# Performance work log

Measured on AMD Instinct MI355X. Metric: run time of the kernel, lower is better.

Reference implementation:

```python
import jax, jax.numpy as jnp
import numpy as np

N = 1_000_000
D_IN = 64
D_HID = 128
NUM_SEG = 8192


def setup_inputs() -> dict:
    key = jax.random.key(0)
    ks = jax.random.split(key, 8)
    f_all = jax.random.normal(ks[0], (N, D_IN), dtype=jnp.float32)
    seg_ids = jnp.sort(jax.random.randint(ks[1], (N,), 0, NUM_SEG, dtype=jnp.int32))
    W1 = jax.random.normal(ks[2], (D_IN, 32), dtype=jnp.float32) * 0.1
    b1 = jax.random.normal(ks[3], (32,), dtype=jnp.float32) * 0.1
    W2 = jax.random.normal(ks[4], (32, 64), dtype=jnp.float32) * 0.1
    b2 = jax.random.normal(ks[5], (64,), dtype=jnp.float32) * 0.1
    W3 = jax.random.normal(ks[6], (64, D_HID), dtype=jnp.float32) * 0.1
    b3 = jax.random.normal(ks[7], (D_HID,), dtype=jnp.float32) * 0.1
    return {"f_all": f_all, "seg_ids": seg_ids, "num_segments": NUM_SEG,
            "W1": W1, "b1": b1, "W2": W2, "b2": b2, "W3": W3, "b3": b3}


def reference(f_all, seg_ids, num_segments, W1, b1, W2, b2, W3, b3):
    # 3-layer MLP: input -> 32 -> 64 -> hidden_size, ReLU on first two
    y = jax.nn.relu(f_all @ W1 + b1)          # [N, 32]
    y = jax.nn.relu(y @ W2 + b2)              # [N, 64]
    y = y @ W3 + b3                           # [N, hidden]
    # per-segment mean; empty segments stay zero (matches torch.zeros init)
    sums = jax.ops.segment_sum(y, seg_ids, num_segments=num_segments)           # [S, hidden]
    counts = jax.ops.segment_sum(jnp.ones((f_all.shape[0],), y.dtype), seg_ids,
                                 num_segments=num_segments)                     # [S]
    return sums / jnp.maximum(counts, 1.0)[:, None]
```

## Files before the change

### kernel.cpp

```cpp
#include <hip/hip_runtime.h>

constexpr int D_IN  = 64;
constexpr int D_H1  = 32;
constexpr int D_H2  = 64;
constexpr int D_OUT = 128;
constexpr int NSEG  = 8192;

constexpr int BLOCK = 256;
constexpr int RT    = 64;
constexpr int TPB   = 8;

typedef __bf16 bfx8 __attribute__((ext_vector_type(8)));
typedef __bf16 bfx4 __attribute__((ext_vector_type(4)));
typedef float  fx4  __attribute__((ext_vector_type(4)));


#define BAR_LGKM() do {                                        \
    asm volatile("s_waitcnt lgkmcnt(0)" ::: "memory");         \
    __builtin_amdgcn_s_barrier();                              \
    __builtin_amdgcn_sched_barrier(0);                         \
} while (0)

__global__ __launch_bounds__(BLOCK, 3) void mlp_seg_mfma(
    const float* __restrict__ f, const int* __restrict__ seg,
    const float* __restrict__ W1, const float* __restrict__ b1,
    const float* __restrict__ W2, const float* __restrict__ b2,
    const float* __restrict__ W3, const float* __restrict__ b3,
    float* __restrict__ sums, float* __restrict__ counts,
    int N, int ntiles)
{
    __shared__ __align__(16) __bf16 sf [2][RT * 64];
    __shared__ __align__(16) __bf16 sh1[RT * 32];
    __shared__ __align__(16) __bf16 sh2[RT * 64];
    __shared__ __align__(16) __bf16 syT[D_OUT * 64];
    __shared__ int sseg[2][RT];

    const int tid  = threadIdx.x;
    const int wv   = tid >> 6;
    const int lane = tid & 63;
    const int lr   = lane & 15;
    const int quad = lane >> 4;
    const int m0   = wv * 16;
    const int ar   = m0 + lr;

    bfx8 fw1[2][2];
    #pragma unroll
    for (int j = 0; j < 2; ++j)
        #pragma unroll
        for (int ks = 0; ks < 2; ++ks)
            #pragma unroll
            for (int i = 0; i < 8; ++i)
                fw1[j][ks][i] = (__bf16)W1[(ks*32 + quad*8 + i)*D_H1 + j*16 + lr];

    bfx8 fw2[4];
    #pragma unroll
    for (int j = 0; j < 4; ++j)
        #pragma unroll
        for (int i = 0; i < 8; ++i)
            fw2[j][i] = (__bf16)W2[(quad*8 + i)*D_H2 + j*16 + lr];

    bfx8 fw3[2][2];
    #pragma unroll
    for (int j = 0; j < 2; ++j)
        #pragma unroll
        for (int ks = 0; ks < 2; ++ks)
            #pragma unroll
            for (int i = 0; i < 8; ++i)
                fw3[j][ks][i] = (__bf16)W3[(ks*32 + quad*8 + i)*D_OUT + wv*32 + j*16 + lr];

    float rb1[2], rb2[4], rb3[2];
    #pragma unroll
    for (int j = 0; j < 2; ++j) rb1[j] = b1[j*16 + lr];
    #pragma unroll
    for (int j = 0; j < 4; ++j) rb2[j] = b2[j*16 + lr];
    #pragma unroll
    for (int j = 0; j < 2; ++j) rb3[j] = b3[wv*32 + j*16 + lr];

    const int colA = tid & 127;
    const int grp  = tid >> 7;
    int   cur_seg = -1;
    float run_sum = 0.f;
    int   run_len = 0;

    const int t0 = blockIdx.x * TPB;
    const int t1 = min(t0 + TPB, ntiles);

    {
        const int R0 = t0 * RT;
        const float4* f4 = (const float4*)f + (size_t)R0 * 16;
        #pragma unroll
        for (int i = 0; i < 4; ++i) {
            const int idx4 = tid + i * 256;
            float4 qq = make_float4(0.f, 0.f, 0.f, 0.f);
            if ((size_t)R0 * 64 + (size_t)idx4 * 4 < (size_t)N * 64) qq = f4[idx4];
            const int r = idx4 >> 4;
            const int c = (idx4 & 15) * 4;
            bfx4 v;
            v[0] = (__bf16)qq.x; v[1] = (__bf16)qq.y;
            v[2] = (__bf16)qq.z; v[3] = (__bf16)qq.w;
            *(bfx4*)&sf[0][r*64 + (((c >> 3) ^ (r & 7)) << 3) + (c & 7)] = v;
        }
        if (tid < RT) sseg[0][tid] = (R0 + tid < N) ? seg[R0 + tid] : -2;
    }
    __syncthreads();

    int p = 0;
    for (int t = t0; t < t1; ++t, p ^= 1) {
        const int R0 = t * RT;
        const bool havenext = (t + 1 < t1);

        float4 q[4];
        int rseg = -2;
        if (havenext) {
            const float4* f4n = (const float4*)f + (size_t)(R0 + RT) * 16;
            #pragma unroll
            for (int i = 0; i < 4; ++i) {
                const int idx4 = tid + i * 256;
                q[i] = make_float4(0.f, 0.f, 0.f, 0.f);
                if ((size_t)(R0 + RT) * 64 + (size_t)idx4 * 4 < (size_t)N * 64)
                    q[i] = f4n[idx4];
            }
            if (tid < RT) rseg = (R0 + RT + tid < N) ? seg[R0 + RT + tid] : -2;
        }

        fx4 acc1[2] = {{0,0,0,0},{0,0,0,0}};
        #pragma unroll
        for (int ks = 0; ks < 2; ++ks) {
            bfx8 a = *(const bfx8*)&sf[p][ar*64 + (((ks*4 + quad) ^ (ar & 7)) << 3)];
            #pragma unroll
            for (int j = 0; j < 2; ++j)
                acc1[j] = __builtin_amdgcn_mfma_f32_16x16x32_bf16(a, fw1[j][ks], acc1[j], 0, 0, 0);
        }
        #pragma unroll
        for (int j = 0; j < 2; ++j)
            #pragma unroll
            for (int rg = 0; rg < 4; ++rg) {
                const int row = m0 + quad*4 + rg;
                const int col = j*16 + lr;
                const float v = fmaxf(acc1[j][rg] + rb1[j], 0.f);
                sh1[row*32 + (((col >> 3) ^ (row & 3)) << 3) + (col & 7)] = (__bf16)v;
            }

        fx4 acc2[4] = {{0,0,0,0},{0,0,0,0},{0,0,0,0},{0,0,0,0}};
        {
            bfx8 a = *(const bfx8*)&sh1[ar*32 + ((quad ^ (ar & 3)) << 3)];
            #pragma unroll
            for (int j = 0; j < 4; ++j)
                acc2[j] = __builtin_amdgcn_mfma_f32_16x16x32_bf16(a, fw2[j], acc2[j], 0, 0, 0);
        }
        #pragma unroll
        for (int j = 0; j < 4; ++j)
            #pragma unroll
            for (int rg = 0; rg < 4; ++rg) {
                const int row = m0 + quad*4 + rg;
                const int col = j*16 + lr;
                const float v = fmaxf(acc2[j][rg] + rb2[j], 0.f);
                sh2[row*64 + (((col >> 3) ^ (row & 7)) << 3) + (col & 7)] = (__bf16)v;
            }

        BAR_LGKM();

        #pragma unroll
        for (int mt = 0; mt < 4; ++mt) {
            fx4 acc3[2] = {{0,0,0,0},{0,0,0,0}};
            const int arow = mt*16 + lr;
            #pragma unroll
            for (int ks = 0; ks < 2; ++ks) {
                bfx8 a = *(const bfx8*)&sh2[arow*64 + (((ks*4 + quad) ^ (arow & 7)) << 3)];
                #pragma unroll
                for (int j = 0; j < 2; ++j)
                    acc3[j] = __builtin_amdgcn_mfma_f32_16x16x32_bf16(a, fw3[j][ks], acc3[j], 0, 0, 0);
            }
            #pragma unroll
            for (int j = 0; j < 2; ++j) {
                bfx4 w;
                #pragma unroll
                for (int rg = 0; rg < 4; ++rg)
                    w[rg] = (__bf16)(acc3[j][rg] + rb3[j]);
                const int col  = wv*32 + j*16 + lr;
                const int row0 = mt*16 + quad*4;
                *(bfx4*)&syT[col*64 + (((row0 >> 3) ^ (col & 7)) << 3) + (quad & 1)*4] = w;
            }
        }

        if (havenext) {
            __bf16* sfn = sf[p ^ 1];
            #pragma unroll
            for (int i = 0; i < 4; ++i) {
                const int idx4 = tid + i * 256;
                const int r = idx4 >> 4;
                const int c = (idx4 & 15) * 4;
                bfx4 v;
                v[0] = (__bf16)q[i].x; v[1] = (__bf16)q[i].y;
                v[2] = (__bf16)q[i].z; v[3] = (__bf16)q[i].w;
                *(bfx4*)&sfn[r*64 + (((c >> 3) ^ (r & 7)) << 3) + (c & 7)] = v;
            }
            if (tid < RT) sseg[p ^ 1][tid] = rseg;
        }

        BAR_LGKM();

        #pragma unroll
        for (int ch = 0; ch < 4; ++ch) {
            const int r8 = grp*32 + ch*8;
            const bfx8 v8 = *(const bfx8*)&syT[colA*64 + (((grp*4 + ch) ^ (colA & 7)) << 3)];
            const int sA = sseg[p][r8];
            const int sB = sseg[p][r8 + 7];
            if (sA == sB) {
                float sum = 0.f;
                #pragma unroll
                for (int k = 0; k < 8; ++k) sum += (float)v8[k];
                if (sA != cur_seg) {
                    if (cur_seg >= 0) {
                        atomicAdd(&sums[(size_t)cur_seg * D_OUT + colA], run_sum);
                        if (colA == 0) atomicAdd(&counts[cur_seg], (float)run_len);
                    }
                    cur_seg = sA; run_sum = sum; run_len = 8;
                } else {
                    run_sum += sum; run_len += 8;
                }
            } else {
                #pragma unroll
                for (int k = 0; k < 8; ++k) {
                    const int s = sseg[p][r8 + k];
                    if (s != cur_seg) {
                        if (cur_seg >= 0) {
                            atomicAdd(&sums[(size_t)cur_seg * D_OUT + colA], run_sum);
                            if (colA == 0) atomicAdd(&counts[cur_seg], (float)run_len);
                        }
                        cur_seg = s; run_sum = 0.f; run_len = 0;
                    }
                    run_sum += (float)v8[k]; run_len++;
                }
            }
        }
    }

    if (cur_seg >= 0) {
        atomicAdd(&sums[(size_t)cur_seg * D_OUT + colA], run_sum);
        if (colA == 0) atomicAdd(&counts[cur_seg], (float)run_len);
    }
}

__global__ __launch_bounds__(256) void div_kernel(
    const float* __restrict__ sums, const float* __restrict__ counts,
    float* __restrict__ out, int total)
{
    const int i = blockIdx.x * 256 + threadIdx.x;
    if (i < total) out[i] = sums[i] / fmaxf(counts[i >> 7], 1.f);
}

extern "C" void kernel_launch(void* const* d_in, const int* in_sizes, int n_in,
                              void* d_out, int out_size, void* d_ws, size_t ws_size,
                              hipStream_t stream) {
    const float* f   = (const float*)d_in[0];
    const int*   seg = (const int*)  d_in[1];
    const float* W1 = (const float*)d_in[3];
    const float* b1 = (const float*)d_in[4];
    const float* W2 = (const float*)d_in[5];
    const float* b2 = (const float*)d_in[6];
    const float* W3 = (const float*)d_in[7];
    const float* b3 = (const float*)d_in[8];
    float* out = (float*)d_out;

    const int N = in_sizes[0] / D_IN;

    float* sums   = (float*)d_ws;
    float* counts = sums + (size_t)NSEG * D_OUT;

    hipMemsetAsync(d_ws, 0, ((size_t)NSEG * D_OUT + NSEG) * sizeof(float), stream);

    const int ntiles  = (N + RT - 1) / RT;
    const int nblocks = (ntiles + TPB - 1) / TPB;
    mlp_seg_mfma<<<nblocks, BLOCK, 0, stream>>>(f, seg, W1, b1, W2, b2, W3, b3,
                                                sums, counts, N, ntiles);

    const int total = NSEG * D_OUT;
    div_kernel<<<(total + 255) / 256, 256, 0, stream>>>(sums, counts, out, total);
}
```

Measured before the change: 401.6 us.

## Single-buffer input tile, transpose MFMA operands for vector LDS stores, raise occupancy

Drops the double-buffered input tile in LDS in favour of one buffer. The next tile is still prefetched into registers, and it is now written after layer 1 has finished reading the buffer. The MFMA operands for layers 1 and 2 are swapped so each lane holds 4 consecutive output columns of one row, which allows packed bfx4 stores to LDS in place of scattered scalar stores. Launch bounds go from 3 to 4 blocks per CU to use the LDS that was freed. The cost is tighter register limits, which could cause spills, and bias values loaded per lane.

Measured after the change: 511.0 us. 1.27x slower.

```diff
diff --git a/kernel.cpp b/kernel.cpp
--- a/kernel.cpp
+++ b/kernel.cpp
@@ -21,7 +21,7 @@
     __builtin_amdgcn_sched_barrier(0);                         \
 } while (0)
 
-__global__ __launch_bounds__(BLOCK, 3) void mlp_seg_mfma(
+__global__ __launch_bounds__(BLOCK, 4) void mlp_seg_mfma(
     const float* __restrict__ f, const int* __restrict__ seg,
     const float* __restrict__ W1, const float* __restrict__ b1,
     const float* __restrict__ W2, const float* __restrict__ b2,
@@ -29,7 +29,7 @@
     float* __restrict__ sums, float* __restrict__ counts,
     int N, int ntiles)
 {
-    __shared__ __align__(16) __bf16 sf [2][RT * 64];
+    __shared__ __align__(16) __bf16 sf [RT * 64];
     __shared__ __align__(16) __bf16 sh1[RT * 32];
     __shared__ __align__(16) __bf16 sh2[RT * 64];
     __shared__ __align__(16) __bf16 syT[D_OUT * 64];
@@ -68,11 +68,16 @@
             for (int i = 0; i < 8; ++i)
                 fw3[j][ks][i] = (__bf16)W3[(ks*32 + quad*8 + i)*D_OUT + wv*32 + j*16 + lr];
 
-    float rb1[2], rb2[4], rb3[2];
-    #pragma unroll
-    for (int j = 0; j < 2; ++j) rb1[j] = b1[j*16 + lr];
-    #pragma unroll
-    for (int j = 0; j < 4; ++j) rb2[j] = b2[j*16 + lr];
+    fx4 rb1v[2], rb2v[4];
+    #pragma unroll
+    for (int j = 0; j < 2; ++j)
+        #pragma unroll
+        for (int rg = 0; rg < 4; ++rg) rb1v[j][rg] = b1[j*16 + quad*4 + rg];
+    #pragma unroll
+    for (int j = 0; j < 4; ++j)
+        #pragma unroll
+        for (int rg = 0; rg < 4; ++rg) rb2v[j][rg] = b2[j*16 + quad*4 + rg];
+    float rb3[2];
     #pragma unroll
     for (int j = 0; j < 2; ++j) rb3[j] = b3[wv*32 + j*16 + lr];
 
@@ -98,7 +103,7 @@
             bfx4 v;
             v[0] = (__bf16)qq.x; v[1] = (__bf16)qq.y;
             v[2] = (__bf16)qq.z; v[3] = (__bf16)qq.w;
-            *(bfx4*)&sf[0][r*64 + (((c >> 3) ^ (r & 7)) << 3) + (c & 7)] = v;
+            *(bfx4*)&sf[r*64 + (((c >> 3) ^ (r & 7)) << 3) + (c & 7)] = v;
         }
         if (tid < RT) sseg[0][tid] = (R0 + tid < N) ? seg[R0 + tid] : -2;
     }
@@ -126,37 +131,37 @@
         fx4 acc1[2] = {{0,0,0,0},{0,0,0,0}};
         #pragma unroll
         for (int ks = 0; ks < 2; ++ks) {
-            bfx8 a = *(const bfx8*)&sf[p][ar*64 + (((ks*4 + quad) ^ (ar & 7)) << 3)];
+            bfx8 a = *(const bfx8*)&sf[ar*64 + (((ks*4 + quad) ^ (ar & 7)) << 3)];
             #pragma unroll
             for (int j = 0; j < 2; ++j)
-                acc1[j] = __builtin_amdgcn_mfma_f32_16x16x32_bf16(a, fw1[j][ks], acc1[j], 0, 0, 0);
-        }
-        #pragma unroll
-        for (int j = 0; j < 2; ++j)
-            #pragma unroll
-            for (int rg = 0; rg < 4; ++rg) {
-                const int row = m0 + quad*4 + rg;
-                const int col = j*16 + lr;
-                const float v = fmaxf(acc1[j][rg] + rb1[j], 0.f);
-                sh1[row*32 + (((col >> 3) ^ (row & 3)) << 3) + (col & 7)] = (__bf16)v;
-            }
+                acc1[j] = __builtin_amdgcn_mfma_f32_16x16x32_bf16(fw1[j][ks], a, acc1[j], 0, 0, 0);
+        }
+        #pragma unroll
+        for (int j = 0; j < 2; ++j) {
+            bfx4 w;
+            #pragma unroll
+            for (int rg = 0; rg < 4; ++rg)
+                w[rg] = (__bf16)fmaxf(acc1[j][rg] + rb1v[j][rg], 0.f);
+            const int b = j*2 + (quad >> 1);
+            *(bfx4*)&sh1[ar*32 + ((b ^ (ar & 3)) << 3) + (quad & 1)*4] = w;
+        }
 
         fx4 acc2[4] = {{0,0,0,0},{0,0,0,0},{0,0,0,0},{0,0,0,0}};
         {
             bfx8 a = *(const bfx8*)&sh1[ar*32 + ((quad ^ (ar & 3)) << 3)];
             #pragma unroll
             for (int j = 0; j < 4; ++j)
-                acc2[j] = __builtin_amdgcn_mfma_f32_16x16x32_bf16(a, fw2[j], acc2[j], 0, 0, 0);
-        }
-        #pragma unroll
-        for (int j = 0; j < 4; ++j)
-            #pragma unroll
-            for (int rg = 0; rg < 4; ++rg) {
-                const int row = m0 + quad*4 + rg;
-                const int col = j*16 + lr;
-                const float v = fmaxf(acc2[j][rg] + rb2[j], 0.f);
-                sh2[row*64 + (((col >> 3) ^ (row & 7)) << 3) + (col & 7)] = (__bf16)v;
-            }
+                acc2[j] = __builtin_amdgcn_mfma_f32_16x16x32_bf16(fw2[j], a, acc2[j], 0, 0, 0);
+        }
+        #pragma unroll
+        for (int j = 0; j < 4; ++j) {
+            bfx4 w;
+            #pragma unroll
+            for (int rg = 0; rg < 4; ++rg)
+                w[rg] = (__bf16)fmaxf(acc2[j][rg] + rb2v[j][rg], 0.f);
+            const int b = j*2 + (quad >> 1);
+            *(bfx4*)&sh2[ar*64 + ((b ^ (ar & 7)) << 3) + (quad & 1)*4] = w;
+        }
 
         BAR_LGKM();
 
@@ -184,7 +189,6 @@
         }
 
         if (havenext) {
-            __bf16* sfn = sf[p ^ 1];
             #pragma unroll
             for (int i = 0; i < 4; ++i) {
                 const int idx4 = tid + i * 256;
@@ -193,7 +197,7 @@
                 bfx4 v;
                 v[0] = (__bf16)q[i].x; v[1] = (__bf16)q[i].y;
                 v[2] = (__bf16)q[i].z; v[3] = (__bf16)q[i].w;
-                *(bfx4*)&sfn[r*64 + (((c >> 3) ^ (r & 7)) << 3) + (c & 7)] = v;
+                *(bfx4*)&sf[r*64 + (((c >> 3) ^ (r & 7)) << 3) + (c & 7)] = v;
             }
             if (tid < RT) sseg[p ^ 1][tid] = rseg;
         }
```
